# Kernel optimization log

Measured on AMD Instinct MI355X. Metric: run time of the kernel, lower is better.

Reference implementation:

```python
import jax, jax.numpy as jnp
import numpy as np
import math

DIM = 1024
HEADS = 16
HEAD_DIM = DIM // HEADS
SCALE = math.sqrt(HEAD_DIM)


def setup_inputs() -> dict:
    key = jax.random.key(0)
    ks = jax.random.split(key, 7)
    B, T, C = 2, 2048, DIM
    w = 0.02
    return {
        "x": jax.random.normal(ks[0], (B, T, C), dtype=jnp.float32),
        "W_Q": jax.random.normal(ks[1], (C, C), dtype=jnp.float32) * w,
        "W_K": jax.random.normal(ks[2], (C, C), dtype=jnp.float32) * w,
        "W_V": jax.random.normal(ks[3], (C, C), dtype=jnp.float32) * w,
        "W_K_prime": jax.random.normal(ks[4], (C, C), dtype=jnp.float32) * w,
        "W_O": jax.random.normal(ks[5], (C, C), dtype=jnp.float32) * w,
        "alpha": jnp.float32(0.5),
    }


def _heads(y, B, T):
    # (B,T,C) -> (B,H,T,D)
    return y.reshape(B, T, HEADS, HEAD_DIM).transpose(0, 2, 1, 3)


def reference(x, W_Q, W_K, W_V, W_K_prime, W_O, alpha):
    B, T, C = x.shape
    # nn.Linear(no bias): y = x @ W.T
    q = _heads(x @ W_Q.T, B, T)
    k = _heads(x @ W_K.T, B, T)
    v = _heads(x @ W_V.T, B, T)
    kp = _heads(x @ W_K_prime.T, B, T)

    # Standard branch
    scores = jnp.einsum("bhqd,bhkd->bhqk", q, k) / SCALE
    attn = jax.nn.softmax(scores, axis=-1)  # dropout = identity (eval mode)
    out_std = jnp.einsum("bhqk,bhkd->bhqd", attn, v)

    # K' branch
    scores_p = jnp.einsum("bhqd,bhkd->bhqk", q, kp) / SCALE
    attn_p = jax.nn.softmax(scores_p, axis=-1)
    out_p = jnp.einsum("bhqk,bhkd->bhqd", attn_p, v)

    out = alpha * out_std + (1.0 - alpha) * out_p
    out = out.transpose(0, 2, 1, 3).reshape(B, T, C)
    return out @ W_O.T
```

## Files before the change

### kernel.cpp

```cpp
#include <hip/hip_runtime.h>
#include <math.h>

#define TSZ 2048
#define CDIM 1024

typedef __attribute__((ext_vector_type(8))) short s16x8;
typedef __attribute__((ext_vector_type(4))) float f32x4;
typedef __attribute__((ext_vector_type(16))) float f32x16;
typedef __attribute__((ext_vector_type(2))) unsigned int u32x2;
typedef __attribute__((ext_vector_type(4))) unsigned int u32x4;

#define QSCL 0.1803368801f

__device__ __forceinline__ short f2bf(float f) {
    union { float f; unsigned u; } v; v.f = f;
    unsigned r = v.u + 0x7fffu + ((v.u >> 16) & 1u);
    return (short)(r >> 16);
}
__device__ __forceinline__ unsigned cvtpk(float lo, float hi) {
    unsigned r;
    asm("v_cvt_pk_bf16_f32 %0, %1, %2" : "=v"(r) : "v"(lo), "v"(hi));
    return r;
}
__device__ __forceinline__ float fexp2(float x) {
    float r;
    asm("v_exp_f32 %0, %1" : "=v"(r) : "v"(x));
    return r;
}
__device__ __forceinline__ s16x8 u2s(u32x4 u) {
    union { u32x4 u; s16x8 s; } c; c.u = u; return c.s;
}
__device__ __forceinline__ f32x16 mfma32(s16x8 a, s16x8 b, f32x16 c) {
    return __builtin_amdgcn_mfma_f32_32x32x16_bf16(a, b, c, 0, 0, 0);
}

__global__ void cast_all(const float* __restrict__ x,
                         const float* __restrict__ w0, const float* __restrict__ w1,
                         const float* __restrict__ w2, const float* __restrict__ w3,
                         const float* __restrict__ w4,
                         short* __restrict__ xb,
                         short* __restrict__ o0, short* __restrict__ o1,
                         short* __restrict__ o2, short* __restrict__ o3,
                         short* __restrict__ o4) {
    int z = blockIdx.y;
    int i = blockIdx.x * blockDim.x + threadIdx.x;
    if (z == 0) {
        for (int j = i; j < (TSZ * 2 * CDIM) / 4; j += 1024 * 256) {
            float4 v = reinterpret_cast<const float4*>(x)[j];
            short4 o;
            o.x = f2bf(v.x); o.y = f2bf(v.y); o.z = f2bf(v.z); o.w = f2bf(v.w);
            reinterpret_cast<short4*>(xb)[j] = o;
        }
    } else {
        const float* s = z == 1 ? w0 : z == 2 ? w1 : z == 3 ? w2 : z == 4 ? w3 : w4;
        short* d = z == 1 ? o0 : z == 2 ? o1 : z == 3 ? o2 : z == 4 ? o3 : o4;
        float4 v = reinterpret_cast<const float4*>(s)[i];
        short4 o;
        o.x = f2bf(v.x); o.y = f2bf(v.y); o.z = f2bf(v.z); o.w = f2bf(v.w);
        reinterpret_cast<short4*>(d)[i] = o;
    }
}

__device__ __forceinline__ void gload16(const short* g, short* l) {
    __builtin_amdgcn_global_load_lds((const __attribute__((address_space(1))) void*)g,
                                     (__attribute__((address_space(3))) void*)l, 16, 0, 0);
}

__device__ __forceinline__ void stage128x64(short* lds_t, const short* g, int ld, int tid, int w) {
    #pragma unroll
    for (int call = 0; call < 4; ++call) {
        int c = call * 256 + tid;
        int row = c >> 3;
        int sc = (c & 7) ^ (row & 7);
        gload16(g + (size_t)row * ld + sc * 8, lds_t + (size_t)(call * 256 + w * 64) * 8);
    }
}

__device__ __forceinline__ void stage64x64(short* lds_t, const short* g, int ld, int tid, int w) {
    #pragma unroll
    for (int call = 0; call < 2; ++call) {
        int c = call * 256 + tid;
        int row = c >> 3;
        int sc = (c & 7) ^ (row & 7);
        gload16(g + (size_t)row * ld + sc * 8, lds_t + (size_t)(call * 256 + w * 64) * 8);
    }
}

__device__ __forceinline__ s16x8 frag_read(const short* tile, int row, int kc) {
    const char* p = (const char*)tile + row * 128 + (((kc ^ (row & 7)) & 7) << 4);
    return *reinterpret_cast<const s16x8*>(p);
}

__global__ __launch_bounds__(256) void gemm4_proj(
    const short* __restrict__ xb,
    const short* __restrict__ w0, const short* __restrict__ w1,
    const short* __restrict__ w2, const short* __restrict__ w3,
    short* __restrict__ o0, short* __restrict__ o1,
    short* __restrict__ o2, short* __restrict__ o3)
{
    __shared__ short sA[128 * 64], sB[128 * 64];
    int tid = threadIdx.x, lane = tid & 63, w = tid >> 6;
    int h = lane >> 5, l31 = lane & 31;
    int wrow = w >> 1, wcol = w & 1;
    int z = blockIdx.y;
    const short* W = z == 0 ? w0 : z == 1 ? w1 : z == 2 ? w2 : w3;
    short* outp = z == 0 ? o0 : z == 1 ? o1 : z == 2 ? o2 : o3;
    int bx = blockIdx.x;
    bx = (bx & 7) * 32 + (bx >> 3);
    int r0 = (bx >> 3) * 128;
    int c0 = (bx & 7) * 128;

    f32x16 acc[2][2];
    #pragma unroll
    for (int i = 0; i < 2; ++i)
        #pragma unroll
        for (int j = 0; j < 2; ++j)
            #pragma unroll
            for (int r = 0; r < 16; ++r) acc[i][j][r] = 0.f;

    for (int kt = 0; kt < 16; ++kt) {
        __syncthreads();
        stage128x64(sA, xb + (size_t)r0 * CDIM + kt * 64, CDIM, tid, w);
        stage128x64(sB, W + (size_t)c0 * CDIM + kt * 64, CDIM, tid, w);
        __syncthreads();
        #pragma unroll
        for (int s = 0; s < 4; ++s) {
            s16x8 af0 = frag_read(sA, wrow * 64 + l31,      2 * s + h);
            s16x8 af1 = frag_read(sA, wrow * 64 + 32 + l31, 2 * s + h);
            s16x8 bf0 = frag_read(sB, wcol * 64 + l31,      2 * s + h);
            s16x8 bf1 = frag_read(sB, wcol * 64 + 32 + l31, 2 * s + h);
            acc[0][0] = mfma32(af0, bf0, acc[0][0]);
            acc[0][1] = mfma32(af0, bf1, acc[0][1]);
            acc[1][0] = mfma32(af1, bf0, acc[1][0]);
            acc[1][1] = mfma32(af1, bf1, acc[1][1]);
        }
    }

    bool vt_mode = (z == 2);
    float oscale = (z == 0) ? QSCL : 1.0f;
    #pragma unroll
    for (int mt = 0; mt < 2; ++mt)
        #pragma unroll
        for (int nt = 0; nt < 2; ++nt)
            #pragma unroll
            for (int r = 0; r < 16; ++r) {
                int gi = r0 + wrow * 64 + mt * 32 + (r & 3) + 8 * (r >> 2) + 4 * h;
                int gn = c0 + wcol * 64 + nt * 32 + l31;
                short v = f2bf(acc[mt][nt][r] * oscale);
                int b = gi >> 11, t = gi & 2047, hh = gn >> 6, d = gn & 63;
                size_t off;
                if (!vt_mode) off = ((size_t)(b * 16 + hh) * TSZ + t) * 64 + d;
                else          off = ((size_t)(b * 16 + hh) * 64 + d) * TSZ + t;
                outp[off] = v;
            }
}

__global__ __launch_bounds__(256) void gemm_final(
    const short* __restrict__ ab, const short* __restrict__ wo, float* __restrict__ out)
{
    __shared__ short sA[128 * 64], sB[128 * 64];
    int tid = threadIdx.x, lane = tid & 63, w = tid >> 6;
    int h = lane >> 5, l31 = lane & 31;
    int wrow = w >> 1, wcol = w & 1;
    int bx = blockIdx.x;
    bx = (bx & 7) * 32 + (bx >> 3);
    int r0 = (bx >> 3) * 128;
    int c0 = (bx & 7) * 128;

    f32x16 acc[2][2];
    #pragma unroll
    for (int i = 0; i < 2; ++i)
        #pragma unroll
        for (int j = 0; j < 2; ++j)
            #pragma unroll
            for (int r = 0; r < 16; ++r) acc[i][j][r] = 0.f;

    for (int kt = 0; kt < 16; ++kt) {
        __syncthreads();
        stage128x64(sA, ab + (size_t)r0 * CDIM + kt * 64, CDIM, tid, w);
        stage128x64(sB, wo + (size_t)c0 * CDIM + kt * 64, CDIM, tid, w);
        __syncthreads();
        #pragma unroll
        for (int s = 0; s < 4; ++s) {
            s16x8 af0 = frag_read(sA, wrow * 64 + l31,      2 * s + h);
            s16x8 af1 = frag_read(sA, wrow * 64 + 32 + l31, 2 * s + h);
            s16x8 bf0 = frag_read(sB, wcol * 64 + l31,      2 * s + h);
            s16x8 bf1 = frag_read(sB, wcol * 64 + 32 + l31, 2 * s + h);
            acc[0][0] = mfma32(af0, bf0, acc[0][0]);
            acc[0][1] = mfma32(af0, bf1, acc[0][1]);
            acc[1][0] = mfma32(af1, bf0, acc[1][0]);
            acc[1][1] = mfma32(af1, bf1, acc[1][1]);
        }
    }

    #pragma unroll
    for (int mt = 0; mt < 2; ++mt)
        #pragma unroll
        for (int nt = 0; nt < 2; ++nt)
            #pragma unroll
            for (int r = 0; r < 16; ++r) {
                int gi = r0 + wrow * 64 + mt * 32 + (r & 3) + 8 * (r >> 2) + 4 * h;
                int gn = c0 + wcol * 64 + nt * 32 + l31;
                out[(size_t)gi * CDIM + gn] = acc[mt][nt][r];
            }
}

__global__ __launch_bounds__(256, 2) void attn_fused(
    const short* __restrict__ q, const short* __restrict__ k, const short* __restrict__ kp,
    const short* __restrict__ vt, const float* __restrict__ alphap, short* __restrict__ aout)
{
    __shared__ short sbuf[6][64 * 64];
    int tid = threadIdx.x, lane = tid & 63, w = tid >> 6;
    int h = lane >> 5, l31 = lane & 31;
    int qg = w >> 1, br = w & 1;

    int id = blockIdx.x + gridDim.x * blockIdx.y;
    int nid = (id & 7) * 64 + (id >> 3);
    int bh = nid >> 4;
    int qt0 = (nid & 15) * 128;

    const short* Q   = q  + (size_t)bh * TSZ * 64;
    const short* Kg  = k  + (size_t)bh * TSZ * 64;
    const short* Kpg = kp + (size_t)bh * TSZ * 64;
    const short* Vt  = vt + (size_t)bh * 64 * TSZ;

    s16x8 qf[2][4];
    #pragma unroll
    for (int qb = 0; qb < 2; ++qb)
        #pragma unroll
        for (int s = 0; s < 4; ++s)
            qf[qb][s] = *reinterpret_cast<const s16x8*>(
                Q + (size_t)(qt0 + qg * 64 + qb * 32 + l31) * 64 + s * 16 + h * 8);

    f32x16 o[2][2];
    #pragma unroll
    for (int qb = 0; qb < 2; ++qb)
        #pragma unroll
        for (int dt = 0; dt < 2; ++dt)
            #pragma unroll
            for (int r = 0; r < 16; ++r) o[qb][dt][r] = 0.f;
    float lloc[2] = {0.f, 0.f};

    stage64x64(sbuf[0], Kg, 64, tid, w);
    stage64x64(sbuf[2], Kpg, 64, tid, w);
    stage64x64(sbuf[4], Vt, TSZ, tid, w);
    __syncthreads();

    int cur = 0;
    for (int kt = 0; kt < 32; ++kt) {
        if (kt < 31) {
            int t0n = (kt + 1) * 64;
            stage64x64(sbuf[cur ^ 1],       Kg  + (size_t)t0n * 64, 64, tid, w);
            stage64x64(sbuf[2 + (cur ^ 1)], Kpg + (size_t)t0n * 64, 64, tid, w);
            stage64x64(sbuf[4 + (cur ^ 1)], Vt + t0n, TSZ, tid, w);
        }
        const short* kbuf = br ? sbuf[2 + cur] : sbuf[cur];
        const short* vbuf = sbuf[4 + cur];

        f32x16 sa[2][2];
        #pragma unroll
        for (int qb = 0; qb < 2; ++qb)
            #pragma unroll
            for (int hf = 0; hf < 2; ++hf)
                #pragma unroll
                for (int r = 0; r < 16; ++r) sa[qb][hf][r] = 0.f;
        __builtin_amdgcn_s_setprio(1);
        #pragma unroll
        for (int s = 0; s < 4; ++s) {
            s16x8 af0 = frag_read(kbuf, l31,      2 * s + h);
            s16x8 af1 = frag_read(kbuf, 32 + l31, 2 * s + h);
            sa[0][0] = mfma32(af0, qf[0][s], sa[0][0]);
            sa[0][1] = mfma32(af1, qf[0][s], sa[0][1]);
            sa[1][0] = mfma32(af0, qf[1][s], sa[1][0]);
            sa[1][1] = mfma32(af1, qf[1][s], sa[1][1]);
        }
        __builtin_amdgcn_s_setprio(0);

        u32x4 pfrag[2][4];
        #pragma unroll
        for (int qb = 0; qb < 2; ++qb) {
            float p0 = 0.f, p1 = 0.f, p2 = 0.f, p3 = 0.f;
            #pragma unroll
            for (int r = 0; r < 16; r += 4) {
                sa[qb][0][r]     = fexp2(sa[qb][0][r]);     p0 += sa[qb][0][r];
                sa[qb][0][r + 1] = fexp2(sa[qb][0][r + 1]); p1 += sa[qb][0][r + 1];
                sa[qb][0][r + 2] = fexp2(sa[qb][0][r + 2]); p2 += sa[qb][0][r + 2];
                sa[qb][0][r + 3] = fexp2(sa[qb][0][r + 3]); p3 += sa[qb][0][r + 3];
                sa[qb][1][r]     = fexp2(sa[qb][1][r]);     p0 += sa[qb][1][r];
                sa[qb][1][r + 1] = fexp2(sa[qb][1][r + 1]); p1 += sa[qb][1][r + 1];
                sa[qb][1][r + 2] = fexp2(sa[qb][1][r + 2]); p2 += sa[qb][1][r + 2];
                sa[qb][1][r + 3] = fexp2(sa[qb][1][r + 3]); p3 += sa[qb][1][r + 3];
            }
            lloc[qb] += (p0 + p1) + (p2 + p3);

            #pragma unroll
            for (int t = 0; t < 2; ++t) {
                unsigned pk[8];
                #pragma unroll
                for (int i = 0; i < 8; ++i)
                    pk[i] = cvtpk(sa[qb][t][2 * i], sa[qb][t][2 * i + 1]);
                u32x2 r02 = __builtin_amdgcn_permlane32_swap(pk[0], pk[2], false, false);
                u32x2 r13 = __builtin_amdgcn_permlane32_swap(pk[1], pk[3], false, false);
                u32x2 r46 = __builtin_amdgcn_permlane32_swap(pk[4], pk[6], false, false);
                u32x2 r57 = __builtin_amdgcn_permlane32_swap(pk[5], pk[7], false, false);
                u32x4 fA, fB;
                fA[0] = r02[0]; fA[1] = r13[0]; fA[2] = r02[1]; fA[3] = r13[1];
                fB[0] = r46[0]; fB[1] = r57[0]; fB[2] = r46[1]; fB[3] = r57[1];
                pfrag[qb][2 * t] = fA;
                pfrag[qb][2 * t + 1] = fB;
            }
        }

        __builtin_amdgcn_s_setprio(1);
        #pragma unroll
        for (int s = 0; s < 4; ++s)
            #pragma unroll
            for (int dt = 0; dt < 2; ++dt) {
                s16x8 vf = frag_read(vbuf, dt * 32 + l31, 2 * s + h);
                o[0][dt] = mfma32(vf, u2s(pfrag[0][s]), o[0][dt]);
                o[1][dt] = mfma32(vf, u2s(pfrag[1][s]), o[1][dt]);
            }
        __builtin_amdgcn_s_setprio(0);

        __syncthreads();
        cur ^= 1;
    }

    float alpha = alphap[0];
    float cb = br ? (1.f - alpha) : alpha;
    float inv[2];
    #pragma unroll
    for (int qb = 0; qb < 2; ++qb) {
        float ls = lloc[qb] + __shfl_xor(lloc[qb], 32, 64);
        inv[qb] = cb / ls;
    }

    float* sX = (float*)&sbuf[0][0];
    if (br) {
        #pragma unroll
        for (int qb = 0; qb < 2; ++qb)
            #pragma unroll
            for (int dt = 0; dt < 2; ++dt)
                #pragma unroll
                for (int g = 0; g < 4; ++g) {
                    int qloc = qg * 64 + qb * 32 + l31;
                    int dsw = (dt * 32 + g * 8 + h * 4) ^ ((l31 & 7) << 3);
                    float4 v4;
                    v4.x = o[qb][dt][4 * g + 0] * inv[qb];
                    v4.y = o[qb][dt][4 * g + 1] * inv[qb];
                    v4.z = o[qb][dt][4 * g + 2] * inv[qb];
                    v4.w = o[qb][dt][4 * g + 3] * inv[qb];
                    *reinterpret_cast<float4*>(sX + qloc * 64 + dsw) = v4;
                }
    }
    __syncthreads();
    if (!br) {
        int b = bh >> 4, hh = bh & 15;
        #pragma unroll
        for (int qb = 0; qb < 2; ++qb) {
            int t = qt0 + qg * 64 + qb * 32 + l31;
            size_t rowbase = ((size_t)(b * TSZ + t)) * CDIM + hh * 64;
            #pragma unroll
            for (int dt = 0; dt < 2; ++dt)
                #pragma unroll
                for (int g = 0; g < 4; ++g) {
                    int qloc = qg * 64 + qb * 32 + l31;
                    int dsw = (dt * 32 + g * 8 + h * 4) ^ ((l31 & 7) << 3);
                    float4 p = *reinterpret_cast<const float4*>(sX + qloc * 64 + dsw);
                    short4 v4;
                    v4.x = f2bf(o[qb][dt][4 * g + 0] * inv[qb] + p.x);
                    v4.y = f2bf(o[qb][dt][4 * g + 1] * inv[qb] + p.y);
                    v4.z = f2bf(o[qb][dt][4 * g + 2] * inv[qb] + p.z);
                    v4.w = f2bf(o[qb][dt][4 * g + 3] * inv[qb] + p.w);
                    *reinterpret_cast<short4*>(aout + rowbase + dt * 32 + g * 8 + h * 4) = v4;
                }
        }
    }
}

extern "C" void kernel_launch(void* const* d_in, const int* in_sizes, int n_in,
                              void* d_out, int out_size, void* d_ws, size_t ws_size,
                              hipStream_t stream)
{
    const float* x     = (const float*)d_in[0];
    const float* WQ    = (const float*)d_in[1];
    const float* WK    = (const float*)d_in[2];
    const float* WV    = (const float*)d_in[3];
    const float* WKp   = (const float*)d_in[4];
    const float* WO    = (const float*)d_in[5];
    const float* alpha = (const float*)d_in[6];
    float* out = (float*)d_out;

    char* ws = (char*)d_ws;
    const size_t MB = 1024 * 1024;
    short* xb   = (short*)(ws + 0);
    short* wqb  = (short*)(ws + 8 * MB);
    short* wkb  = (short*)(ws + 10 * MB);
    short* wvb  = (short*)(ws + 12 * MB);
    short* wkpb = (short*)(ws + 14 * MB);
    short* wob  = (short*)(ws + 16 * MB);
    short* qb   = (short*)(ws + 18 * MB);
    short* kb   = (short*)(ws + 26 * MB);
    short* kpb  = (short*)(ws + 34 * MB);
    short* vtb  = (short*)(ws + 42 * MB);
    short* anb  = (short*)(ws + 50 * MB);

    cast_all<<<dim3(1024, 6), 256, 0, stream>>>(x, WQ, WK, WV, WKp, WO,
                                                xb, wqb, wkb, wvb, wkpb, wob);

    gemm4_proj<<<dim3(256, 4), 256, 0, stream>>>(xb, wqb, wkb, wvb, wkpb, qb, kb, vtb, kpb);
    attn_fused<<<dim3(16, 32), 256, 0, stream>>>(qb, kb, kpb, vtb, alpha, anb);
    gemm_final<<<dim3(256), 256, 0, stream>>>(anb, wob, out);
}
```

Before: 158.2 us.

## Double-buffer LDS tiles in projection and output GEMMs to overlap loads

Both GEMM kernels now keep two LDS buffers for the A and B tiles. The next K-slice is staged while MFMAs run on the current one, and each iteration needs one barrier instead of two. The MFMA section is wrapped in s_setprio raises. This hides global-to-LDS load latency behind compute, at the cost of doubling LDS use to 64KB per block, which may lower occupancy.

```diff
diff --git a/kernel.cpp b/kernel.cpp
--- a/kernel.cpp
+++ b/kernel.cpp
@@ -98,7 +98,7 @@
     short* __restrict__ o0, short* __restrict__ o1,
     short* __restrict__ o2, short* __restrict__ o3)
 {
-    __shared__ short sA[128 * 64], sB[128 * 64];
+    __shared__ short sA[2][128 * 64], sB[2][128 * 64];
     int tid = threadIdx.x, lane = tid & 63, w = tid >> 6;
     int h = lane >> 5, l31 = lane & 31;
     int wrow = w >> 1, wcol = w & 1;
@@ -118,22 +118,33 @@
             #pragma unroll
             for (int r = 0; r < 16; ++r) acc[i][j][r] = 0.f;
 
+    stage128x64(sA[0], xb + (size_t)r0 * CDIM, CDIM, tid, w);
+    stage128x64(sB[0], W + (size_t)c0 * CDIM, CDIM, tid, w);
+    __syncthreads();
+
+    int cur = 0;
     for (int kt = 0; kt < 16; ++kt) {
-        __syncthreads();
-        stage128x64(sA, xb + (size_t)r0 * CDIM + kt * 64, CDIM, tid, w);
-        stage128x64(sB, W + (size_t)c0 * CDIM + kt * 64, CDIM, tid, w);
-        __syncthreads();
+        if (kt < 15) {
+            stage128x64(sA[cur ^ 1], xb + (size_t)r0 * CDIM + (kt + 1) * 64, CDIM, tid, w);
+            stage128x64(sB[cur ^ 1], W + (size_t)c0 * CDIM + (kt + 1) * 64, CDIM, tid, w);
+        }
+        const short* a = sA[cur];
+        const short* b = sB[cur];
+        __builtin_amdgcn_s_setprio(1);
         #pragma unroll
         for (int s = 0; s < 4; ++s) {
-            s16x8 af0 = frag_read(sA, wrow * 64 + l31,      2 * s + h);
-            s16x8 af1 = frag_read(sA, wrow * 64 + 32 + l31, 2 * s + h);
-            s16x8 bf0 = frag_read(sB, wcol * 64 + l31,      2 * s + h);
-            s16x8 bf1 = frag_read(sB, wcol * 64 + 32 + l31, 2 * s + h);
+            s16x8 af0 = frag_read(a, wrow * 64 + l31,      2 * s + h);
+            s16x8 af1 = frag_read(a, wrow * 64 + 32 + l31, 2 * s + h);
+            s16x8 bf0 = frag_read(b, wcol * 64 + l31,      2 * s + h);
+            s16x8 bf1 = frag_read(b, wcol * 64 + 32 + l31, 2 * s + h);
             acc[0][0] = mfma32(af0, bf0, acc[0][0]);
             acc[0][1] = mfma32(af0, bf1, acc[0][1]);
             acc[1][0] = mfma32(af1, bf0, acc[1][0]);
             acc[1][1] = mfma32(af1, bf1, acc[1][1]);
         }
+        __builtin_amdgcn_s_setprio(0);
+        __syncthreads();
+        cur ^= 1;
     }
 
     bool vt_mode = (z == 2);
@@ -158,7 +169,7 @@
 __global__ __launch_bounds__(256) void gemm_final(
     const short* __restrict__ ab, const short* __restrict__ wo, float* __restrict__ out)
 {
-    __shared__ short sA[128 * 64], sB[128 * 64];
+    __shared__ short sA[2][128 * 64], sB[2][128 * 64];
     int tid = threadIdx.x, lane = tid & 63, w = tid >> 6;
     int h = lane >> 5, l31 = lane & 31;
     int wrow = w >> 1, wcol = w & 1;
@@ -175,22 +186,33 @@
             #pragma unroll
             for (int r = 0; r < 16; ++r) acc[i][j][r] = 0.f;
 
+    stage128x64(sA[0], ab + (size_t)r0 * CDIM, CDIM, tid, w);
+    stage128x64(sB[0], wo + (size_t)c0 * CDIM, CDIM, tid, w);
+    __syncthreads();
+
+    int cur = 0;
     for (int kt = 0; kt < 16; ++kt) {
-        __syncthreads();
-        stage128x64(sA, ab + (size_t)r0 * CDIM + kt * 64, CDIM, tid, w);
-        stage128x64(sB, wo + (size_t)c0 * CDIM + kt * 64, CDIM, tid, w);
-        __syncthreads();
+        if (kt < 15) {
+            stage128x64(sA[cur ^ 1], ab + (size_t)r0 * CDIM + (kt + 1) * 64, CDIM, tid, w);
+            stage128x64(sB[cur ^ 1], wo + (size_t)c0 * CDIM + (kt + 1) * 64, CDIM, tid, w);
+        }
+        const short* a = sA[cur];
+        const short* b = sB[cur];
+        __builtin_amdgcn_s_setprio(1);
         #pragma unroll
         for (int s = 0; s < 4; ++s) {
-            s16x8 af0 = frag_read(sA, wrow * 64 + l31,      2 * s + h);
-            s16x8 af1 = frag_read(sA, wrow * 64 + 32 + l31, 2 * s + h);
-            s16x8 bf0 = frag_read(sB, wcol * 64 + l31,      2 * s + h);
-            s16x8 bf1 = frag_read(sB, wcol * 64 + 32 + l31, 2 * s + h);
+            s16x8 af0 = frag_read(a, wrow * 64 + l31,      2 * s + h);
+            s16x8 af1 = frag_read(a, wrow * 64 + 32 + l31, 2 * s + h);
+            s16x8 bf0 = frag_read(b, wcol * 64 + l31,      2 * s + h);
+            s16x8 bf1 = frag_read(b, wcol * 64 + 32 + l31, 2 * s + h);
             acc[0][0] = mfma32(af0, bf0, acc[0][0]);
             acc[0][1] = mfma32(af0, bf1, acc[0][1]);
             acc[1][0] = mfma32(af1, bf0, acc[1][0]);
             acc[1][1] = mfma32(af1, bf1, acc[1][1]);
         }
+        __builtin_amdgcn_s_setprio(0);
+        __syncthreads();
+        cur ^= 1;
     }
 
     #pragma unroll
```

Measured after the change: 160.8 us. Within noise of the previous version (+1.6%).
